# Kernel optimization log

Measured on AMD Instinct MI355X. Metric: run time of the kernel, lower is better.

## Reference

```python
import jax, jax.numpy as jnp
import numpy as np

OUT_H = OUT_W = 15      # POOLER_RESOLUTION (template / pooler_z path)
SCALE = 0.0625          # POOLER_SCALES: 1/16 feature stride
SR = 2                  # POOLER_SAMPLING_RATIO
IMG = 1024.0


def setup_inputs() -> dict:
    key = jax.random.key(0)
    k1, k2, k3, k4, k5 = jax.random.split(key, 5)
    x = jax.random.normal(k1, (2, 256, 64, 64), dtype=jnp.float32)
    N = 512
    cx = jax.random.uniform(k2, (N,), minval=32.0, maxval=IMG - 32.0)
    cy = jax.random.uniform(k3, (N,), minval=32.0, maxval=IMG - 32.0)
    wh = jax.random.uniform(k4, (N, 2), minval=32.0, maxval=160.0)
    x1 = jnp.clip(cx - wh[:, 0] / 2, 0.0, IMG - 1)
    x2 = jnp.clip(cx + wh[:, 0] / 2, 0.0, IMG - 1)
    y1 = jnp.clip(cy - wh[:, 1] / 2, 0.0, IMG - 1)
    y2 = jnp.clip(cy + wh[:, 1] / 2, 0.0, IMG - 1)
    boxes = jnp.stack([x1, y1, x2, y2], axis=1).astype(jnp.float32)
    batch_idx = jax.random.randint(k5, (N,), 0, 2, dtype=jnp.int32)
    return {"x": x, "boxes": boxes, "batch_idx": batch_idx}


def _axis_idx(p, size):
    """ROIAlign bilinear index/frac/validity along one axis. p: [N, K] float."""
    valid = (p >= -1.0) & (p <= size)
    p = jnp.clip(p, 0.0, size - 1.0)
    lo = jnp.floor(p).astype(jnp.int32)
    lo = jnp.minimum(lo, size - 1)
    hi = jnp.minimum(lo + 1, size - 1)
    frac = p - lo.astype(p.dtype)  # 0 when lo==size-1 (matches torch clamp)
    return lo, hi, frac, valid


def roi_align(feats, boxes, batch_idx, out_h, out_w, scale, sr):
    B, C, H, W = feats.shape
    b = boxes * scale
    x1, y1, x2, y2 = b[:, 0], b[:, 1], b[:, 2], b[:, 3]
    roi_w = jnp.maximum(x2 - x1, 1.0)
    roi_h = jnp.maximum(y2 - y1, 1.0)
    bin_w = roi_w / out_w
    bin_h = roi_h / out_h
    # sample point k along an axis: start + (k + 0.5)/sr * bin  (k = ph*sr + iy)
    ky = (jnp.arange(out_h * sr, dtype=feats.dtype) + 0.5) / sr
    kx = (jnp.arange(out_w * sr, dtype=feats.dtype) + 0.5) / sr
    ys = y1[:, None] + ky[None, :] * bin_h[:, None]  # [N, out_h*sr]
    xs = x1[:, None] + kx[None, :] * bin_w[:, None]  # [N, out_w*sr]
    ylo, yhi, fy, vy = _axis_idx(ys, H)
    xlo, xhi, fx, vx = _axis_idx(xs, W)
    bi = batch_idx[:, None, None]

    def gather(yi, xi):
        # feats[b, :, y, x] -> [N, out_h*sr, out_w*sr, C]
        return feats[bi, :, yi[:, :, None], xi[:, None, :]]

    wy_lo = (1.0 - fy) * vy
    wy_hi = fy * vy
    wx_lo = (1.0 - fx) * vx
    wx_hi = fx * vx

    def w2(wy, wx):
        return (wy[:, :, None] * wx[:, None, :])[..., None]  # [N,Hs,Ws,1]

    val = (w2(wy_lo, wx_lo) * gather(ylo, xlo)
           + w2(wy_lo, wx_hi) * gather(ylo, xhi)
           + w2(wy_hi, wx_lo) * gather(yhi, xlo)
           + w2(wy_hi, wx_hi) * gather(yhi, xhi))
    N = boxes.shape[0]
    val = val.reshape(N, out_h, sr, out_w, sr, C).mean(axis=(2, 4))
    return jnp.transpose(val, (0, 3, 1, 2))  # [N, C, out_h, out_w]


def reference(x, boxes, batch_idx):
    # EMMFeatureExtractor.forward with sr=None -> pooler_z (template ROIAlign 15x15)
    return roi_align(x, boxes, batch_idx, OUT_H, OUT_W, SCALE, SR)
```

## Files before the change

### kernel.cpp

```cpp
#include <hip/hip_runtime.h>

constexpr int NROI = 512;
constexpr int CCH  = 256;
constexpr int HH   = 64;
constexpr int WWd  = 64;
constexpr int OHh  = 15;
constexpr int OWw  = 15;
constexpr float SCL = 0.0625f;
constexpr int TSTR  = 17;
constexpr int CPB   = 64;
constexpr int KIT   = CPB / 16;

__global__ __launch_bounds__(256, 4)
void roi_align_kernel(const float* __restrict__ x,
                      const float* __restrict__ boxes,
                      const int* __restrict__ bidx,
                      float* __restrict__ out) {
  __shared__ float T[256 * TSTR];
  __shared__ float wx_s[OWw][3];
  __shared__ float wy_s[OHh][3];
  __shared__ int   jb_s[OWw];
  __shared__ int   rb_s[OHh];

  const int roi = blockIdx.x >> 2;
  const int g   = blockIdx.x & 3;
  const int t   = threadIdx.x;

  if (t < 32) {
    const int axis = t >> 4;
    const int o    = t & 15;
    if (o < OHh) {
      const float p1v = boxes[roi * 4 + axis] * SCL;
      const float p2v = boxes[roi * 4 + 2 + axis] * SCL;
      const float sz  = fmaxf(p2v - p1v, 1.0f);
      const float bin = sz * (1.0f / 15.0f);
      int lo[2]; float wl[2], wh[2];
#pragma unroll
      for (int s = 0; s < 2; ++s) {
        float p = p1v + ((float)(2 * o + s) + 0.5f) * 0.5f * bin;
        const float valid = (p >= -1.0f && p <= 64.0f) ? 0.5f : 0.0f;
        p = fminf(fmaxf(p, 0.0f), 63.0f);
        const int l = (int)p;
        const float f = p - (float)l;
        lo[s] = l; wl[s] = (1.0f - f) * valid; wh[s] = f * valid;
      }
      const int base = min(lo[0], WWd - 3);
      float w[3] = {0.f, 0.f, 0.f};
#pragma unroll
      for (int s = 0; s < 2; ++s) {
        const int hi = min(lo[s] + 1, WWd - 1);
        w[lo[s] - base] += wl[s];
        w[hi - base]    += wh[s];
      }
      if (axis == 0) { jb_s[o] = base; wx_s[o][0] = w[0]; wx_s[o][1] = w[1]; wx_s[o][2] = w[2]; }
      else           { rb_s[o] = base; wy_s[o][0] = w[0]; wy_s[o][1] = w[1]; wy_s[o][2] = w[2]; }
    }
  }
  __syncthreads();

  const int r0 = rb_s[0];
  const int R  = rb_s[OHh - 1] + 3 - r0;
  const int bi = bidx[roi];

  const int ow = t & 15;
  const int cs = t >> 4;
  const bool act = (ow < OWw);

  float wy[OHh][3];
#pragma unroll
  for (int oh = 0; oh < OHh; ++oh) {
    wy[oh][0] = wy_s[oh][0]; wy[oh][1] = wy_s[oh][1]; wy[oh][2] = wy_s[oh][2];
  }
  unsigned rp0 = 0, rp1 = 0;
#pragma unroll
  for (int oh = 0; oh < 8; ++oh)  rp0 |= (unsigned)(rb_s[oh] - r0) << (4 * oh);
#pragma unroll
  for (int oh = 8; oh < OHh; ++oh) rp1 |= (unsigned)(rb_s[oh] - r0) << (4 * (oh - 8));

  float ax0 = 0.f, ax1 = 0.f, ax2 = 0.f;
  int jb = 0;
  if (act) { ax0 = wx_s[ow][0]; ax1 = wx_s[ow][1]; ax2 = wx_s[ow][2]; jb = jb_s[ow]; }

  float* Tp = &T[t * TSTR];
  const int NR2 = (R + 1) >> 1;
  constexpr int OSTR = OHh * OWw;

  for (int k = 0; k < KIT; ++k) {
    const int ch = g * CPB + k * 16 + cs;
    const float* fbase = x + ((size_t)(bi * CCH + ch) * HH) * WWd + jb;
    if (act) {
      for (int it = 0; it < NR2; ++it) {
        const int ra  = r0 + 2 * it;
        const int rb2 = min(ra + 1, HH - 1);
        const float* pa = fbase + ra * WWd;
        const float* pb = fbase + rb2 * WWd;
        Tp[2 * it]     = fmaf(pa[0], ax0, fmaf(pa[1], ax1, pa[2] * ax2));
        Tp[2 * it + 1] = fmaf(pb[0], ax0, fmaf(pb[1], ax1, pb[2] * ax2));
      }
      float* obase = out + ((size_t)roi * CCH + ch) * OSTR + ow;
#pragma unroll
      for (int oh = 0; oh < OHh; ++oh) {
        const unsigned rr = (oh < 8) ? ((rp0 >> (4 * oh)) & 15u)
                                     : ((rp1 >> (4 * (oh - 8))) & 15u);
        const float* q = Tp + rr;
        const float v = fmaf(q[0], wy[oh][0], fmaf(q[1], wy[oh][1], q[2] * wy[oh][2]));
        __builtin_nontemporal_store(v, obase + oh * OWw);
      }
    }
  }
}

extern "C" void kernel_launch(void* const* d_in, const int* in_sizes, int n_in,
                              void* d_out, int out_size, void* d_ws, size_t ws_size,
                              hipStream_t stream) {
  const float* x     = (const float*)d_in[0];
  const float* boxes = (const float*)d_in[1];
  const int*   bid   = (const int*)d_in[2];
  float* out = (float*)d_out;
  hipLaunchKernelGGL(roi_align_kernel, dim3(NROI * 4), dim3(256), 0, stream,
                     x, boxes, bid, out);
}
```

Before: 173.3 us.

## Remap threads per wavefront-channel for coalesced row passes and contiguous output stores

Restructures the work so each 64-lane wavefront handles one channel at a time. Lanes split across rows and output columns in the x-pass, then write the 225 outputs of that channel contiguously in the y-pass, using a shared per-output table of y-weights and row offsets. Two channels' intermediate tiles are interleaved to expose more independent loads, and occupancy is raised to 6 blocks per CU. This aims to replace strided per-thread row walks and scattered 15-stride stores with coalesced access. The cost is extra LDS table setup and a second barrier.

```diff
diff --git a/kernel.cpp b/kernel.cpp
--- a/kernel.cpp
+++ b/kernel.cpp
@@ -7,106 +7,120 @@
 constexpr int OHh  = 15;
 constexpr int OWw  = 15;
 constexpr float SCL = 0.0625f;
-constexpr int TSTR  = 17;
-constexpr int CPB   = 64;
-constexpr int KIT   = CPB / 16;
+constexpr int TSTR = 17;
+constexpr int TSZ  = 16 * TSTR;
+constexpr int OSTR = OHh * OWw;
 
-__global__ __launch_bounds__(256, 4)
+__global__ __launch_bounds__(256, 6)
 void roi_align_kernel(const float* __restrict__ x,
                       const float* __restrict__ boxes,
                       const int* __restrict__ bidx,
                       float* __restrict__ out) {
-  __shared__ float T[256 * TSTR];
-  __shared__ float wx_s[OWw][3];
-  __shared__ float wy_s[OHh][3];
-  __shared__ int   jb_s[OWw];
-  __shared__ int   rb_s[OHh];
+  __shared__ float  Ta[4][TSZ];
+  __shared__ float  Tb[4][TSZ];
+  __shared__ float4 ytab[253];
+  __shared__ float  wx_s[OWw][4];
+  __shared__ float  wy_s[OHh][3];
+  __shared__ int    rb_s[OHh];
 
   const int roi = blockIdx.x >> 2;
   const int g   = blockIdx.x & 3;
   const int t   = threadIdx.x;
+  const int w   = t >> 6;
+  const int l   = t & 63;
 
   if (t < 32) {
-    const int axis = t >> 4;
-    const int o    = t & 15;
+    const int axis = t >> 4, o = t & 15;
     if (o < OHh) {
-      const float p1v = boxes[roi * 4 + axis] * SCL;
-      const float p2v = boxes[roi * 4 + 2 + axis] * SCL;
-      const float sz  = fmaxf(p2v - p1v, 1.0f);
-      const float bin = sz * (1.0f / 15.0f);
+      const float p1 = boxes[roi * 4 + axis] * SCL;
+      const float p2 = boxes[roi * 4 + 2 + axis] * SCL;
+      const float bin = fmaxf(p2 - p1, 1.0f) * (1.0f / 15.0f);
       int lo[2]; float wl[2], wh[2];
 #pragma unroll
       for (int s = 0; s < 2; ++s) {
-        float p = p1v + ((float)(2 * o + s) + 0.5f) * 0.5f * bin;
+        float p = p1 + ((float)(2 * o + s) + 0.5f) * 0.5f * bin;
         const float valid = (p >= -1.0f && p <= 64.0f) ? 0.5f : 0.0f;
         p = fminf(fmaxf(p, 0.0f), 63.0f);
-        const int l = (int)p;
-        const float f = p - (float)l;
-        lo[s] = l; wl[s] = (1.0f - f) * valid; wh[s] = f * valid;
+        const int li = (int)p;
+        const float f = p - (float)li;
+        lo[s] = li; wl[s] = (1.0f - f) * valid; wh[s] = f * valid;
       }
       const int base = min(lo[0], WWd - 3);
-      float w[3] = {0.f, 0.f, 0.f};
+      float wv[3] = {0.f, 0.f, 0.f};
 #pragma unroll
       for (int s = 0; s < 2; ++s) {
         const int hi = min(lo[s] + 1, WWd - 1);
-        w[lo[s] - base] += wl[s];
-        w[hi - base]    += wh[s];
+        wv[lo[s] - base] += wl[s];
+        wv[hi - base]    += wh[s];
       }
-      if (axis == 0) { jb_s[o] = base; wx_s[o][0] = w[0]; wx_s[o][1] = w[1]; wx_s[o][2] = w[2]; }
-      else           { rb_s[o] = base; wy_s[o][0] = w[0]; wy_s[o][1] = w[1]; wy_s[o][2] = w[2]; }
+      if (axis == 0) {
+        wx_s[o][0] = wv[0]; wx_s[o][1] = wv[1]; wx_s[o][2] = wv[2];
+        wx_s[o][3] = __int_as_float(base);
+      } else {
+        wy_s[o][0] = wv[0]; wy_s[o][1] = wv[1]; wy_s[o][2] = wv[2];
+        rb_s[o] = base;
+      }
     }
   }
   __syncthreads();
 
   const int r0 = rb_s[0];
   const int R  = rb_s[OHh - 1] + 3 - r0;
+
+  if (t < OSTR) {
+    const int oh = t / 15, ow2 = t - oh * 15;
+    const int rbase = (rb_s[oh] - r0) * TSTR + ow2;
+    ytab[t + (t >> 3)] = make_float4(wy_s[oh][0], wy_s[oh][1], wy_s[oh][2],
+                                     __int_as_float(rbase));
+  }
+  __syncthreads();
+
   const int bi = bidx[roi];
+  const int xq = l / 15;
+  const int xo = l - xq * 15;
+  const float ax0 = wx_s[xo][0], ax1 = wx_s[xo][1], ax2 = wx_s[xo][2];
+  const int jb = __float_as_int(wx_s[xo][3]);
+  const bool xact = (l < 60);
 
-  const int ow = t & 15;
-  const int cs = t >> 4;
-  const bool act = (ow < OWw);
+  float* Taw = Ta[w];
+  float* Tbw = Tb[w];
 
-  float wy[OHh][3];
+  const size_t chan0 = (size_t)(bi * CCH + g * 64 + w * 16);
+  const float* fb0 = x + (chan0 * HH + (size_t)r0) * WWd + jb;
+  float* ob0 = out + (size_t)(roi * CCH + g * 64 + w * 16) * OSTR;
+
+  auto xpass = [&](int k, float* T) {
+    const float* fb = fb0 + (size_t)k * HH * WWd;
+    if (xact) {
 #pragma unroll
-  for (int oh = 0; oh < OHh; ++oh) {
-    wy[oh][0] = wy_s[oh][0]; wy[oh][1] = wy_s[oh][1]; wy[oh][2] = wy_s[oh][2];
-  }
-  unsigned rp0 = 0, rp1 = 0;
-#pragma unroll
-  for (int oh = 0; oh < 8; ++oh)  rp0 |= (unsigned)(rb_s[oh] - r0) << (4 * oh);
-#pragma unroll
-  for (int oh = 8; oh < OHh; ++oh) rp1 |= (unsigned)(rb_s[oh] - r0) << (4 * (oh - 8));
-
-  float ax0 = 0.f, ax1 = 0.f, ax2 = 0.f;
-  int jb = 0;
-  if (act) { ax0 = wx_s[ow][0]; ax1 = wx_s[ow][1]; ax2 = wx_s[ow][2]; jb = jb_s[ow]; }
-
-  float* Tp = &T[t * TSTR];
-  const int NR2 = (R + 1) >> 1;
-  constexpr int OSTR = OHh * OWw;
-
-  for (int k = 0; k < KIT; ++k) {
-    const int ch = g * CPB + k * 16 + cs;
-    const float* fbase = x + ((size_t)(bi * CCH + ch) * HH) * WWd + jb;
-    if (act) {
-      for (int it = 0; it < NR2; ++it) {
-        const int ra  = r0 + 2 * it;
-        const int rb2 = min(ra + 1, HH - 1);
-        const float* pa = fbase + ra * WWd;
-        const float* pb = fbase + rb2 * WWd;
-        Tp[2 * it]     = fmaf(pa[0], ax0, fmaf(pa[1], ax1, pa[2] * ax2));
-        Tp[2 * it + 1] = fmaf(pb[0], ax0, fmaf(pb[1], ax1, pb[2] * ax2));
-      }
-      float* obase = out + ((size_t)roi * CCH + ch) * OSTR + ow;
-#pragma unroll
-      for (int oh = 0; oh < OHh; ++oh) {
-        const unsigned rr = (oh < 8) ? ((rp0 >> (4 * oh)) & 15u)
-                                     : ((rp1 >> (4 * (oh - 8))) & 15u);
-        const float* q = Tp + rr;
-        const float v = fmaf(q[0], wy[oh][0], fmaf(q[1], wy[oh][1], q[2] * wy[oh][2]));
-        __builtin_nontemporal_store(v, obase + oh * OWw);
+      for (int i2 = 0; i2 < 4; ++i2) {
+        const int rr = i2 * 4 + xq;
+        if (rr < R) {
+          const float* p = fb + rr * WWd;
+          T[rr * TSTR + xo] = fmaf(p[0], ax0, fmaf(p[1], ax1, p[2] * ax2));
+        }
       }
     }
+  };
+  auto ypass = [&](int k, const float* T) {
+    float* ob = ob0 + (size_t)k * OSTR;
+#pragma unroll
+    for (int i2 = 0; i2 < 4; ++i2) {
+      const int o = i2 * 64 + l;
+      if (o < OSTR) {
+        const float4 tw = ytab[o + (o >> 3)];
+        const float* q = T + __float_as_int(tw.w);
+        const float v = fmaf(q[0], tw.x, fmaf(q[TSTR], tw.y, q[2 * TSTR] * tw.z));
+        __builtin_nontemporal_store(v, ob + o);
+      }
+    }
+  };
+
+  for (int k = 0; k < 16; k += 2) {
+    xpass(k, Taw);
+    xpass(k + 1, Tbw);
+    ypass(k, Taw);
+    ypass(k + 1, Tbw);
   }
 }
 
```

New measurement: 157.2 us. 1.1x faster.
